# Performance work log

Measured on AMD Instinct MI355X. Metric: run time of the kernel, lower is better.

## Reference

```python
import jax, jax.numpy as jnp
import numpy as np

N, L, H, D = 8, 1024, 16, 64
HD = H * D          # hidden_size = 1024
MLP = 4 * HD        # mlp_dim = 4096
EPS = 1e-5


def _layer_norm(x, g, b):
    mu = jnp.mean(x, axis=-1, keepdims=True)
    var = jnp.var(x, axis=-1, keepdims=True)
    return (x - mu) * jax.lax.rsqrt(var + EPS) * g + b


def setup_inputs() -> dict:
    key = jax.random.key(0)
    ks = jax.random.split(key, 8)
    s_in = 1.0 / np.sqrt(HD)
    s_mlp = 1.0 / np.sqrt(MLP)
    return {
        "x": jax.random.normal(ks[0], (N, L, HD), jnp.float32),
        "ln0_g": jnp.ones((HD,), jnp.float32),
        "ln0_b": jnp.zeros((HD,), jnp.float32),
        "wq": jax.random.normal(ks[1], (HD, HD), jnp.float32) * s_in,
        "bq": jnp.zeros((HD,), jnp.float32),
        "wk": jax.random.normal(ks[2], (HD, HD), jnp.float32) * s_in,
        "bk": jnp.zeros((HD,), jnp.float32),
        "wv": jax.random.normal(ks[3], (HD, HD), jnp.float32) * s_in,
        "bv": jnp.zeros((HD,), jnp.float32),
        "wo": jax.random.normal(ks[4], (HD, HD), jnp.float32) * s_in,
        "bo": jnp.zeros((HD,), jnp.float32),
        "ln1_g": jnp.ones((HD,), jnp.float32),
        "ln1_b": jnp.zeros((HD,), jnp.float32),
        "w1": jax.random.normal(ks[5], (HD, MLP), jnp.float32) * s_in,
        "b1": jnp.zeros((MLP,), jnp.float32),
        "w2": jax.random.normal(ks[6], (MLP, HD), jnp.float32) * s_mlp,
        "b2": jnp.zeros((HD,), jnp.float32),
    }


def reference(x, ln0_g, ln0_b, wq, bq, wk, bk, wv, bv, wo, bo,
              ln1_g, ln1_b, w1, b1, w2, b2):
    n, l, hd = x.shape
    # --- pre-LN self-attention ---
    y = _layer_norm(x, ln0_g, ln0_b)
    q = (y @ wq + bq).reshape(n, l, H, D)
    k = (y @ wk + bk).reshape(n, l, H, D)
    v = (y @ wv + bv).reshape(n, l, H, D)
    qkt = jnp.einsum('nqhd,nkhd->nqkh', q, k) / jnp.sqrt(jnp.float32(D))
    attn = jax.nn.softmax(qkt, axis=2)
    y = jnp.einsum('nqkh,nkhd->nqhd', attn, v).reshape(n, l, hd)
    y = y @ wo + bo
    x = x + y  # residual (dropout_rate=0 in eval)
    # --- pre-LN MLP ---
    y = _layer_norm(x, ln1_g, ln1_b)
    y = jax.nn.gelu(y @ w1 + b1)
    y = y @ w2 + b2
    return x + y
```

## Files before the change

### kernel.cpp

```cpp
#include <hip/hip_runtime.h>
#include <math.h>

typedef __attribute__((ext_vector_type(8))) __bf16 bf16x8;
typedef __attribute__((ext_vector_type(4))) float f32x4;

#define NBATCH 8
#define SEQ    1024
#define NHEAD  16
#define DHEAD  64
#define HID    1024
#define MLPD   4096

static __device__ __forceinline__ unsigned short f2bf(float f) {
  unsigned int u = __float_as_uint(f);
  u += 0x7fffu + ((u >> 16) & 1u);
  return (unsigned short)(u >> 16);
}

static __device__ __forceinline__ void gload_lds16(const unsigned short* g,
                                                   unsigned short* l) {
  __builtin_amdgcn_global_load_lds(
      (const __attribute__((address_space(1))) unsigned int*)g,
      (__attribute__((address_space(3))) unsigned int*)l, 16, 0, 0);
}

static __device__ __forceinline__ float gelu_fast(float v) {
  const float z = 0.7978845608028654f * (v + 0.044715f * v * v * v);
  const float e = __expf(-2.0f * fabsf(z));
  float th = (1.0f - e) / (1.0f + e);
  th = copysignf(th, z);
  return 0.5f * v * (1.0f + th);
}

#define MFMA16(a, b, c) __builtin_amdgcn_mfma_f32_16x16x32_bf16(a, b, c, 0, 0, 0)

__global__ __launch_bounds__(256) void k_prep(const float* __restrict__ wq,
                                              const float* __restrict__ wk,
                                              const float* __restrict__ wv,
                                              const float* __restrict__ wo,
                                              const float* __restrict__ w1,
                                              const float* __restrict__ w2,
                                              const float* __restrict__ bq,
                                              const float* __restrict__ bk,
                                              const float* __restrict__ bv,
                                              unsigned short* __restrict__ qkvT,
                                              unsigned short* __restrict__ woT,
                                              unsigned short* __restrict__ w1T,
                                              unsigned short* __restrict__ w2T,
                                              float* __restrict__ bqkv) {
  __shared__ float t[32][33];
  const int b = blockIdx.x;
  const float* in;
  unsigned short* out;
  int R, C, ti;
  if (b < 4096) {
    const int m = b >> 10;
    ti = b & 1023; R = 1024; C = 1024;
    in  = (m == 0) ? wq : (m == 1) ? wk : (m == 2) ? wv : wo;
    out = (m == 3) ? woT : qkvT + (size_t)m * 1024 * 1024;
  } else if (b < 8192) {
    ti = b - 4096; R = 1024; C = 4096; in = w1; out = w1T;
  } else if (b < 12288) {
    ti = b - 8192; R = 4096; C = 1024; in = w2; out = w2T;
  } else {
    const int i = (b - 12288) * 256 + threadIdx.x;
    if (i < 3 * HID)
      bqkv[i] = (i < HID) ? bq[i] : (i < 2 * HID ? bk[i - HID] : bv[i - 2 * HID]);
    return;
  }
  const int tpr = C >> 5;
  const int c0 = (ti % tpr) * 32, r0 = (ti / tpr) * 32;
  const int tx = threadIdx.x & 31, ty = threadIdx.x >> 5;
#pragma unroll
  for (int j = 0; j < 4; ++j)
    t[ty + j * 8][tx] = in[(size_t)(r0 + ty + j * 8) * C + c0 + tx];
  __syncthreads();
#pragma unroll
  for (int j = 0; j < 4; ++j)
    out[(size_t)(c0 + ty + j * 8) * R + r0 + tx] = f2bf(t[tx][ty + j * 8]);
}

__global__ __launch_bounds__(256) void k_ln(const float* __restrict__ x,
                                            const float* __restrict__ gw,
                                            const float* __restrict__ bw,
                                            unsigned short* __restrict__ y) {
  __shared__ float red[2][4];
  const int row = blockIdx.x;
  const int tid = threadIdx.x;
  const float4 v = ((const float4*)(x + (size_t)row * HID))[tid];
  float sum = v.x + v.y + v.z + v.w;
  float sq  = v.x * v.x + v.y * v.y + v.z * v.z + v.w * v.w;
#pragma unroll
  for (int off = 32; off >= 1; off >>= 1) {
    sum += __shfl_xor(sum, off);
    sq  += __shfl_xor(sq, off);
  }
  if ((tid & 63) == 0) { red[0][tid >> 6] = sum; red[1][tid >> 6] = sq; }
  __syncthreads();
  sum = red[0][0] + red[0][1] + red[0][2] + red[0][3];
  sq  = red[1][0] + red[1][1] + red[1][2] + red[1][3];
  const float mu  = sum * (1.0f / HID);
  const float var = sq * (1.0f / HID) - mu * mu;
  const float rs  = rsqrtf(var + 1e-5f);
  const float4 g4 = ((const float4*)gw)[tid];
  const float4 b4 = ((const float4*)bw)[tid];
  ushort4 ov;
  ov.x = f2bf((v.x - mu) * rs * g4.x + b4.x);
  ov.y = f2bf((v.y - mu) * rs * g4.y + b4.y);
  ov.z = f2bf((v.z - mu) * rs * g4.z + b4.z);
  ov.w = f2bf((v.w - mu) * rs * g4.w + b4.w);
  ((ushort4*)(y + (size_t)row * HID))[tid] = ov;
}

template <int EPI, int BN>
__global__ __launch_bounds__(512, 2) void k_gemm(const unsigned short* __restrict__ A,
                                                 const unsigned short* __restrict__ BT,
                                                 const float* __restrict__ bias,
                                                 const float* __restrict__ res,
                                                 void* __restrict__ Cout,
                                                 int M, int N, int K) {
  constexpr int ASZ = 256 * 64;
  constexpr int BSZ = BN * 64;
  constexpr int NF  = BN / 64;
  constexpr int NCW = BN / 4;
  __shared__ unsigned short sh[2 * ASZ + 2 * BSZ];

  const int tid  = threadIdx.x;
  const int lane = tid & 63;
  const int w    = tid >> 6;
  const int wr   = w >> 2, wc = w & 3;
  const int l15  = lane & 15, g = lane >> 4;

  const int gx = gridDim.x;
  const int nwg = gx * gridDim.y;
  int lid = blockIdx.y * gx + blockIdx.x;
  lid = (lid & 7) * (nwg >> 3) + (lid >> 3);
  const int m0 = (lid / gx) * 256, n0 = (lid % gx) * BN;

  f32x4 acc[8][NF] = {};

  const int srow  = w * 8 + (lane >> 3);
  const int scolb = ((lane & 7) * 16) ^ (((lane >> 3) & 7) << 4);
  const unsigned short* pA = A  + (size_t)(m0 + srow) * K + (scolb >> 1);
  const unsigned short* pB = BT + (size_t)(n0 + srow) * K + (scolb >> 1);
  unsigned short* shB = sh + 2 * ASZ;

#define STAGE(buf_, kk)                                                     \
  do {                                                                      \
    _Pragma("unroll") for (int c = 0; c < 4; ++c)                           \
      gload_lds16(pA + (size_t)c * 64 * K + (kk),                           \
                  sh + (buf_) * ASZ + (c * 64 + w * 8) * 64);               \
    _Pragma("unroll") for (int c = 0; c < BN / 64; ++c)                     \
      gload_lds16(pB + (size_t)c * 64 * K + (kk),                           \
                  shB + (buf_) * BSZ + (c * 64 + w * 8) * 64);              \
  } while (0)

  const int fmask = (l15 & 7) << 4;
  const int bo0 = ((0 * 64) + g * 16) ^ fmask;
  const int bo1 = ((1 * 64) + g * 16) ^ fmask;
  const int aRowBase = wr * 128 + l15;
  const int bRowBase = wc * NCW + l15;

  const int NT = K >> 6;

  STAGE(0, 0);
  int buf = 0;
  for (int t = 0; t < NT; ++t) {
    const unsigned short* shAb = sh + buf * ASZ;
    const unsigned short* shBb = shB + buf * BSZ;

    asm volatile("s_waitcnt vmcnt(0)" ::: "memory");
    __builtin_amdgcn_sched_barrier(0);
    __builtin_amdgcn_s_barrier();
    if (t + 1 < NT) STAGE(buf ^ 1, (t + 1) * 64);

    bf16x8 bfr[NF][2];
#pragma unroll
    for (int n = 0; n < NF; ++n) {
      const int br = (bRowBase + n * 16) * 64;
      bfr[n][0] = *(const bf16x8*)(shBb + br + (bo0 >> 1));
      bfr[n][1] = *(const bf16x8*)(shBb + br + (bo1 >> 1));
    }
    bf16x8 afr[8][2];
#pragma unroll
    for (int m = 0; m < 8; ++m) {
      const int ar = (aRowBase + m * 16) * 64;
      afr[m][0] = *(const bf16x8*)(shAb + ar + (bo0 >> 1));
      afr[m][1] = *(const bf16x8*)(shAb + ar + (bo1 >> 1));
    }
    __builtin_amdgcn_sched_barrier(0);

#pragma unroll
    for (int p = 0; p < 4; ++p) {
#pragma unroll
      for (int n = 0; n < NF; ++n) {
        acc[2 * p][n]     = MFMA16(afr[2 * p][0],     bfr[n][0], acc[2 * p][n]);
        acc[2 * p][n]     = MFMA16(afr[2 * p][1],     bfr[n][1], acc[2 * p][n]);
        acc[2 * p + 1][n] = MFMA16(afr[2 * p + 1][0], bfr[n][0], acc[2 * p + 1][n]);
        acc[2 * p + 1][n] = MFMA16(afr[2 * p + 1][1], bfr[n][1], acc[2 * p + 1][n]);
      }
    }
    buf ^= 1;
  }
#undef STAGE

  if constexpr (EPI == 2) {
#pragma unroll
    for (int m = 0; m < 8; ++m) {
#pragma unroll
      for (int n = 0; n < NF; ++n) {
        const int col = n0 + wc * NCW + n * 16 + l15;
        const float bc = bias[col];
#pragma unroll
        for (int r = 0; r < 4; ++r) {
          const int row = m0 + wr * 128 + m * 16 + g * 4 + r;
          const size_t idx = (size_t)row * N + col;
          ((float*)Cout)[idx] = acc[m][n][r] + bc + res[idx];
        }
      }
    }
  } else {
    __builtin_amdgcn_s_barrier();
    unsigned short* ep = sh + w * (128 * NCW);
#pragma unroll
    for (int m = 0; m < 8; ++m) {
#pragma unroll
      for (int n = 0; n < NF; ++n) {
        const float bc = bias[n0 + wc * NCW + n * 16 + l15];
#pragma unroll
        for (int r = 0; r < 4; ++r) {
          float v = acc[m][n][r] + bc;
          if constexpr (EPI == 1) v = gelu_fast(v);
          ep[(m * 16 + g * 4 + r) * NCW + n * 16 + l15] = f2bf(v);
        }
      }
    }
    constexpr int CPR = NCW / 8;
#pragma unroll
    for (int j = 0; j < NCW / 4; ++j) {
      const int t = lane + j * 64;
      const int row = t / CPR, colb = (t % CPR) * 8;
      const uint4 vv = *(const uint4*)(ep + row * NCW + colb);
      unsigned short* outp = (unsigned short*)Cout +
          (size_t)(m0 + wr * 128 + row) * N + n0 + wc * NCW + colb;
      *(uint4*)outp = vv;
    }
  }
}

__global__ __launch_bounds__(256) void k_vt(const unsigned short* __restrict__ qkv,
                                            unsigned short* __restrict__ vT) {
  __shared__ unsigned short t[64][72];
  const int nh = blockIdx.y;
  const int nb = nh >> 4, h = nh & 15;
  const int l0 = blockIdx.x * 64;
  const int tx = threadIdx.x & 7;
  const int ty = threadIdx.x >> 3;
  const unsigned short* src = qkv + (size_t)(nb * SEQ + l0) * 3072 + 2048 + h * DHEAD;
#pragma unroll
  for (int j = 0; j < 2; ++j)
    *(uint4*)(&t[ty + j * 32][tx * 8]) =
        *(const uint4*)(&src[(size_t)(ty + j * 32) * 3072 + tx * 8]);
  __syncthreads();
  unsigned short* dst = vT + (size_t)nh * DHEAD * SEQ + l0;
#pragma unroll
  for (int j = 0; j < 2; ++j) {
    const int d = ty + j * 32;
    ushort4 a, b;
    a.x = t[tx * 8 + 0][d]; a.y = t[tx * 8 + 1][d];
    a.z = t[tx * 8 + 2][d]; a.w = t[tx * 8 + 3][d];
    b.x = t[tx * 8 + 4][d]; b.y = t[tx * 8 + 5][d];
    b.z = t[tx * 8 + 6][d]; b.w = t[tx * 8 + 7][d];
    *(ushort4*)(&dst[(size_t)d * SEQ + tx * 8])     = a;
    *(ushort4*)(&dst[(size_t)d * SEQ + tx * 8 + 4]) = b;
  }
}

#define SOFTMAX_GROUP(S, gq)                                                       \
  {                                                                                \
    float mx = -INFINITY;                                                          \
    _Pragma("unroll") for (int c = 0; c < 4; ++c)                                  \
      _Pragma("unroll") for (int r = 0; r < 4; ++r)                                \
        mx = fmaxf(mx, S[c][r]);                                                   \
    mx = fmaxf(mx, __shfl_xor(mx, 16));                                            \
    mx = fmaxf(mx, __shfl_xor(mx, 32));                                            \
    const float mnew = fmaxf(m_run[gq], mx);                                       \
    const float sc = __expf(0.125f * (m_run[gq] - mnew));                          \
    m_run[gq] = mnew;                                                              \
    float ts = 0.0f;                                                               \
    _Pragma("unroll") for (int c = 0; c < 4; ++c) {                                \
      const float p0 = __expf(0.125f * (S[c][0] - mnew));                          \
      const float p1 = __expf(0.125f * (S[c][1] - mnew));                          \
      const float p2 = __expf(0.125f * (S[c][2] - mnew));                          \
      const float p3 = __expf(0.125f * (S[c][3] - mnew));                          \
      ts += (p0 + p1) + (p2 + p3);                                                 \
      const unsigned int lo = (unsigned int)f2bf(p0) | ((unsigned int)f2bf(p1) << 16); \
      const unsigned int hi = (unsigned int)f2bf(p2) | ((unsigned int)f2bf(p3) << 16); \
      *(uint2*)(&P_lds[w][((gq) * 16 + l15) * 72 + c * 16 + g * 4]) = make_uint2(lo, hi); \
    }                                                                              \
    ts += __shfl_xor(ts, 16);                                                      \
    ts += __shfl_xor(ts, 32);                                                      \
    s_run[gq] = s_run[gq] * sc + ts;                                               \
    const float scr0 = __shfl(sc, g * 4 + 0), scr1 = __shfl(sc, g * 4 + 1);        \
    const float scr2 = __shfl(sc, g * 4 + 2), scr3 = __shfl(sc, g * 4 + 3);        \
    _Pragma("unroll") for (int dt = 0; dt < 4; ++dt) {                             \
      o[gq][dt][0] *= scr0; o[gq][dt][1] *= scr1;                                  \
      o[gq][dt][2] *= scr2; o[gq][dt][3] *= scr3;                                  \
    }                                                                              \
  }

__global__ __launch_bounds__(256, 4) void k_attn(const unsigned short* __restrict__ qkv,
                                                 const unsigned short* __restrict__ vT,
                                                 unsigned short* __restrict__ outp) {
  __shared__ unsigned short Ks[64 * 64];
  __shared__ unsigned short Vs[64 * 64];
  __shared__ unsigned short P_lds[4][32 * 72];
  const int tid  = threadIdx.x;
  const int lane = tid & 63;
  const int w    = tid >> 6;
  const int l15  = lane & 15, g = lane >> 4;
  const int nh = blockIdx.y;
  const int nb = nh >> 4, h = nh & 15;
  const int q0 = blockIdx.x * 128 + w * 32;
  const size_t RS = 3 * HID;

  const unsigned short* Qp = qkv + (size_t)(nb * SEQ + q0) * RS + h * DHEAD;
  const unsigned short* Kg = qkv + (size_t)(nb * SEQ) * RS + HID + h * DHEAD;
  const unsigned short* Vg = vT + (size_t)nh * DHEAD * SEQ;

  const int L0 = tid * 32, L1 = L0 + 16;
  const int kr0 = L0 >> 7, kc0 = (L0 & 127) ^ ((kr0 & 7) << 4);
  const int kr1 = L1 >> 7, kc1 = (L1 & 127) ^ ((kr1 & 7) << 4);

  bf16x8 aq[2][2];
#pragma unroll
  for (int gq = 0; gq < 2; ++gq)
#pragma unroll
    for (int t = 0; t < 2; ++t)
      aq[gq][t] = *(const bf16x8*)(&Qp[(size_t)(gq * 16 + l15) * RS + t * 32 + g * 8]);

  f32x4 o[2][4] = {};
  float m_run[2] = {-INFINITY, -INFINITY};
  float s_run[2] = {0.0f, 0.0f};

  uint4 rk0, rk1, rv0, rv1;
  rk0 = *(const uint4*)(Kg + (size_t)kr0 * RS + (kc0 >> 1));
  rk1 = *(const uint4*)(Kg + (size_t)kr1 * RS + (kc1 >> 1));
  rv0 = *(const uint4*)(Vg + (size_t)kr0 * SEQ + (kc0 >> 1));
  rv1 = *(const uint4*)(Vg + (size_t)kr1 * SEQ + (kc1 >> 1));
  *(uint4*)(&Ks[tid * 16])     = rk0;
  *(uint4*)(&Ks[tid * 16 + 8]) = rk1;
  *(uint4*)(&Vs[tid * 16])     = rv0;
  *(uint4*)(&Vs[tid * 16 + 8]) = rv1;
  __syncthreads();

  const int sw = (l15 & 7) << 4;

  for (int t16 = 0; t16 < 16; ++t16) {
    if (t16 < 15) {
      const int kb = (t16 + 1) * 64;
      rk0 = *(const uint4*)(Kg + (size_t)(kb + kr0) * RS + (kc0 >> 1));
      rk1 = *(const uint4*)(Kg + (size_t)(kb + kr1) * RS + (kc1 >> 1));
      rv0 = *(const uint4*)(Vg + (size_t)kr0 * SEQ + kb + (kc0 >> 1));
      rv1 = *(const uint4*)(Vg + (size_t)kr1 * SEQ + kb + (kc1 >> 1));
    }

    f32x4 S0[4], S1[4];
#pragma unroll
    for (int c = 0; c < 4; ++c) {
      const int krow = c * 16 + l15;
      const bf16x8 k0 = *(const bf16x8*)(&Ks[krow * 64 + ((( 0 + g * 16) ^ sw) >> 1)]);
      const bf16x8 k1 = *(const bf16x8*)(&Ks[krow * 64 + (((64 + g * 16) ^ sw) >> 1)]);
      f32x4 a = {};
      a = MFMA16(k0, aq[0][0], a);
      a = MFMA16(k1, aq[0][1], a);
      S0[c] = a;
      f32x4 b = {};
      b = MFMA16(k0, aq[1][0], b);
      b = MFMA16(k1, aq[1][1], b);
      S1[c] = b;
    }

    SOFTMAX_GROUP(S0, 0)
    SOFTMAX_GROUP(S1, 1)

    bf16x8 pa[2][2];
#pragma unroll
    for (int gq = 0; gq < 2; ++gq)
#pragma unroll
      for (int th = 0; th < 2; ++th)
        pa[gq][th] = *(const bf16x8*)(&P_lds[w][(gq * 16 + l15) * 72 + th * 32 + g * 8]);
#pragma unroll
    for (int dt = 0; dt < 4; ++dt) {
      const int vrow = dt * 16 + l15;
      const bf16x8 v0 = *(const bf16x8*)(&Vs[vrow * 64 + ((( 0 + g * 16) ^ sw) >> 1)]);
      const bf16x8 v1 = *(const bf16x8*)(&Vs[vrow * 64 + (((64 + g * 16) ^ sw) >> 1)]);
      o[0][dt] = MFMA16(pa[0][0], v0, o[0][dt]);
      o[0][dt] = MFMA16(pa[0][1], v1, o[0][dt]);
      o[1][dt] = MFMA16(pa[1][0], v0, o[1][dt]);
      o[1][dt] = MFMA16(pa[1][1], v1, o[1][dt]);
    }
    __syncthreads();
    if (t16 < 15) {
      *(uint4*)(&Ks[tid * 16])     = rk0;
      *(uint4*)(&Ks[tid * 16 + 8]) = rk1;
      *(uint4*)(&Vs[tid * 16])     = rv0;
      *(uint4*)(&Vs[tid * 16 + 8]) = rv1;
      __syncthreads();
    }
  }

#pragma unroll
  for (int gq = 0; gq < 2; ++gq) {
    float sr[4];
#pragma unroll
    for (int r = 0; r < 4; ++r) sr[r] = 1.0f / __shfl(s_run[gq], g * 4 + r);
#pragma unroll
    for (int dt = 0; dt < 4; ++dt)
#pragma unroll
      for (int r = 0; r < 4; ++r)
        outp[(size_t)(nb * SEQ + q0 + gq * 16 + g * 4 + r) * HID + h * DHEAD + dt * 16 + l15] =
            f2bf(o[gq][dt][r] * sr[r]);
  }
}

extern "C" void kernel_launch(void* const* d_in, const int* in_sizes, int n_in,
                              void* d_out, int out_size, void* d_ws, size_t ws_size,
                              hipStream_t stream) {
  const float* x    = (const float*)d_in[0];
  const float* ln0g = (const float*)d_in[1];
  const float* ln0b = (const float*)d_in[2];
  const float* wq   = (const float*)d_in[3];
  const float* bq   = (const float*)d_in[4];
  const float* wk   = (const float*)d_in[5];
  const float* bk   = (const float*)d_in[6];
  const float* wv   = (const float*)d_in[7];
  const float* bv   = (const float*)d_in[8];
  const float* wo   = (const float*)d_in[9];
  const float* bo   = (const float*)d_in[10];
  const float* ln1g = (const float*)d_in[11];
  const float* ln1b = (const float*)d_in[12];
  const float* w1   = (const float*)d_in[13];
  const float* b1   = (const float*)d_in[14];
  const float* w2   = (const float*)d_in[15];
  const float* b2   = (const float*)d_in[16];
  float* out = (float*)d_out;

  char* ws = (char*)d_ws;
  unsigned short* qkvT = (unsigned short*)(ws + 0);
  unsigned short* woT  = (unsigned short*)(ws + 6291456);
  unsigned short* w1T  = (unsigned short*)(ws + 8388608);
  unsigned short* w2T  = (unsigned short*)(ws + 16777216);
  float*          bqkv = (float*)(ws + 25165824);
  unsigned short* ybuf = (unsigned short*)(ws + 25178112);
  unsigned short* qkv  = (unsigned short*)(ws + 41955328);
  unsigned short* att  = (unsigned short*)(ws + 92286976);
  unsigned short* hbuf = qkv;
  unsigned short* vT   = ybuf;

  const int M = NBATCH * SEQ;

  k_prep<<<dim3(12300), 256, 0, stream>>>(wq, wk, wv, wo, w1, w2, bq, bk, bv,
                                          qkvT, woT, w1T, w2T, bqkv);

  k_ln<<<dim3(M), 256, 0, stream>>>(x, ln0g, ln0b, ybuf);
  k_gemm<0, 256><<<dim3(12, 32), 512, 0, stream>>>(ybuf, qkvT, bqkv, nullptr, (void*)qkv, M, 3 * HID, HID);
  k_vt<<<dim3(16, 128), 256, 0, stream>>>(qkv, vT);
  k_attn<<<dim3(8, 128), 256, 0, stream>>>(qkv, vT, att);
  k_gemm<2, 128><<<dim3(8, 32), 512, 0, stream>>>(att, woT, bo, x, (void*)out, M, HID, HID);
  k_ln<<<dim3(M), 256, 0, stream>>>(out, ln1g, ln1b, ybuf);
  k_gemm<1, 256><<<dim3(16, 32), 512, 0, stream>>>(ybuf, w1T, b1, nullptr, (void*)hbuf, M, MLPD, HID);
  k_gemm<2, 128><<<dim3(8, 32), 512, 0, stream>>>(hbuf, w2T, b2, out, (void*)out, M, HID, MLPD);
}
```

Baseline: 363.6 us.

## Shrink GEMM tiles to 256x128 with K-step 32 for higher occupancy

The GEMM kernel now uses a fixed 256x128 output tile and a K-step of 32 instead of 64, which cuts shared memory per block and raises the launch-bounds occupancy target from 2 to 4 blocks. The swizzled LDS staging, fragment loads and epilogue staging are rewritten to match, with the epilogue split into two 64-row halves. The QKV and MLP-up grids double in the N direction. The aim is more resident workgroups to hide latency, at the cost of less data reuse per tile and twice as many barrier/load iterations along K.

```diff
diff --git a/kernel.cpp b/kernel.cpp
--- a/kernel.cpp
+++ b/kernel.cpp
@@ -112,17 +112,18 @@
   ((ushort4*)(y + (size_t)row * HID))[tid] = ov;
 }
 
-template <int EPI, int BN>
-__global__ __launch_bounds__(512, 2) void k_gemm(const unsigned short* __restrict__ A,
+template <int EPI>
+__global__ __launch_bounds__(512, 4) void k_gemm(const unsigned short* __restrict__ A,
                                                  const unsigned short* __restrict__ BT,
                                                  const float* __restrict__ bias,
                                                  const float* __restrict__ res,
                                                  void* __restrict__ Cout,
                                                  int M, int N, int K) {
-  constexpr int ASZ = 256 * 64;
-  constexpr int BSZ = BN * 64;
-  constexpr int NF  = BN / 64;
-  constexpr int NCW = BN / 4;
+  constexpr int BN  = 128;
+  constexpr int ASZ = 256 * 32;
+  constexpr int BSZ = BN * 32;
+  constexpr int NF  = 2;
+  constexpr int NCW = 32;
   __shared__ unsigned short sh[2 * ASZ + 2 * BSZ];
 
   const int tid  = threadIdx.x;
@@ -139,29 +140,24 @@
 
   f32x4 acc[8][NF] = {};
 
-  const int srow  = w * 8 + (lane >> 3);
-  const int scolb = ((lane & 7) * 16) ^ (((lane >> 3) & 7) << 4);
-  const unsigned short* pA = A  + (size_t)(m0 + srow) * K + (scolb >> 1);
-  const unsigned short* pB = BT + (size_t)(n0 + srow) * K + (scolb >> 1);
+  const int srow4 = lane >> 2;
+  const int schk  = (lane & 3) ^ ((lane >> 3) & 3);
+  const unsigned short* pA = A  + (size_t)(m0 + w * 32 + srow4) * K + schk * 8;
+  const unsigned short* pB = BT + (size_t)(n0 + w * 16 + srow4) * K + schk * 8;
   unsigned short* shB = sh + 2 * ASZ;
 
-#define STAGE(buf_, kk)                                                     \
-  do {                                                                      \
-    _Pragma("unroll") for (int c = 0; c < 4; ++c)                           \
-      gload_lds16(pA + (size_t)c * 64 * K + (kk),                           \
-                  sh + (buf_) * ASZ + (c * 64 + w * 8) * 64);               \
-    _Pragma("unroll") for (int c = 0; c < BN / 64; ++c)                     \
-      gload_lds16(pB + (size_t)c * 64 * K + (kk),                           \
-                  shB + (buf_) * BSZ + (c * 64 + w * 8) * 64);              \
+#define STAGE(buf_, kk)                                                      \
+  do {                                                                       \
+    gload_lds16(pA + (kk),                  sh  + (buf_) * ASZ + (w * 32) * 32);      \
+    gload_lds16(pA + (size_t)16 * K + (kk), sh  + (buf_) * ASZ + (w * 32 + 16) * 32); \
+    gload_lds16(pB + (kk),                  shB + (buf_) * BSZ + (w * 16) * 32);      \
   } while (0)
 
-  const int fmask = (l15 & 7) << 4;
-  const int bo0 = ((0 * 64) + g * 16) ^ fmask;
-  const int bo1 = ((1 * 64) + g * 16) ^ fmask;
+  const int fko = (g ^ ((l15 >> 1) & 3)) * 8;
   const int aRowBase = wr * 128 + l15;
   const int bRowBase = wc * NCW + l15;
 
-  const int NT = K >> 6;
+  const int NT = K >> 5;
 
   STAGE(0, 0);
   int buf = 0;
@@ -172,32 +168,24 @@
     asm volatile("s_waitcnt vmcnt(0)" ::: "memory");
     __builtin_amdgcn_sched_barrier(0);
     __builtin_amdgcn_s_barrier();
-    if (t + 1 < NT) STAGE(buf ^ 1, (t + 1) * 64);
-
-    bf16x8 bfr[NF][2];
-#pragma unroll
-    for (int n = 0; n < NF; ++n) {
-      const int br = (bRowBase + n * 16) * 64;
-      bfr[n][0] = *(const bf16x8*)(shBb + br + (bo0 >> 1));
-      bfr[n][1] = *(const bf16x8*)(shBb + br + (bo1 >> 1));
-    }
-    bf16x8 afr[8][2];
-#pragma unroll
-    for (int m = 0; m < 8; ++m) {
-      const int ar = (aRowBase + m * 16) * 64;
-      afr[m][0] = *(const bf16x8*)(shAb + ar + (bo0 >> 1));
-      afr[m][1] = *(const bf16x8*)(shAb + ar + (bo1 >> 1));
-    }
+    if (t + 1 < NT) STAGE(buf ^ 1, (t + 1) * 32);
+
+    bf16x8 bfr[NF];
+#pragma unroll
+    for (int n = 0; n < NF; ++n)
+      bfr[n] = *(const bf16x8*)(shBb + (bRowBase + n * 16) * 32 + fko);
+    bf16x8 afr[8];
+#pragma unroll
+    for (int m = 0; m < 8; ++m)
+      afr[m] = *(const bf16x8*)(shAb + (aRowBase + m * 16) * 32 + fko);
     __builtin_amdgcn_sched_barrier(0);
 
 #pragma unroll
     for (int p = 0; p < 4; ++p) {
 #pragma unroll
       for (int n = 0; n < NF; ++n) {
-        acc[2 * p][n]     = MFMA16(afr[2 * p][0],     bfr[n][0], acc[2 * p][n]);
-        acc[2 * p][n]     = MFMA16(afr[2 * p][1],     bfr[n][1], acc[2 * p][n]);
-        acc[2 * p + 1][n] = MFMA16(afr[2 * p + 1][0], bfr[n][0], acc[2 * p + 1][n]);
-        acc[2 * p + 1][n] = MFMA16(afr[2 * p + 1][1], bfr[n][1], acc[2 * p + 1][n]);
+        acc[2 * p][n]     = MFMA16(afr[2 * p],     bfr[n], acc[2 * p][n]);
+        acc[2 * p + 1][n] = MFMA16(afr[2 * p + 1], bfr[n], acc[2 * p + 1][n]);
       }
     }
     buf ^= 1;
@@ -221,29 +209,32 @@
     }
   } else {
     __builtin_amdgcn_s_barrier();
-    unsigned short* ep = sh + w * (128 * NCW);
-#pragma unroll
-    for (int m = 0; m < 8; ++m) {
-#pragma unroll
-      for (int n = 0; n < NF; ++n) {
-        const float bc = bias[n0 + wc * NCW + n * 16 + l15];
-#pragma unroll
-        for (int r = 0; r < 4; ++r) {
-          float v = acc[m][n][r] + bc;
-          if constexpr (EPI == 1) v = gelu_fast(v);
-          ep[(m * 16 + g * 4 + r) * NCW + n * 16 + l15] = f2bf(v);
+    unsigned short* ep = sh + w * (64 * NCW);
+#pragma unroll
+    for (int hm = 0; hm < 2; ++hm) {
+#pragma unroll
+      for (int m = 0; m < 4; ++m) {
+        const int mm = hm * 4 + m;
+#pragma unroll
+        for (int n = 0; n < NF; ++n) {
+          const float bc = bias[n0 + wc * NCW + n * 16 + l15];
+#pragma unroll
+          for (int r = 0; r < 4; ++r) {
+            float v = acc[mm][n][r] + bc;
+            if constexpr (EPI == 1) v = gelu_fast(v);
+            ep[(m * 16 + g * 4 + r) * NCW + n * 16 + l15] = f2bf(v);
+          }
         }
       }
-    }
-    constexpr int CPR = NCW / 8;
-#pragma unroll
-    for (int j = 0; j < NCW / 4; ++j) {
-      const int t = lane + j * 64;
-      const int row = t / CPR, colb = (t % CPR) * 8;
-      const uint4 vv = *(const uint4*)(ep + row * NCW + colb);
-      unsigned short* outp = (unsigned short*)Cout +
-          (size_t)(m0 + wr * 128 + row) * N + n0 + wc * NCW + colb;
-      *(uint4*)outp = vv;
+#pragma unroll
+      for (int j = 0; j < 4; ++j) {
+        const int t = lane + j * 64;
+        const int row = t >> 2, colb = (t & 3) * 8;
+        const uint4 vv = *(const uint4*)(ep + row * NCW + colb);
+        unsigned short* outp = (unsigned short*)Cout +
+            (size_t)(m0 + wr * 128 + hm * 64 + row) * N + n0 + wc * NCW + colb;
+        *(uint4*)outp = vv;
+      }
     }
   }
 }
@@ -464,11 +455,11 @@
                                           qkvT, woT, w1T, w2T, bqkv);
 
   k_ln<<<dim3(M), 256, 0, stream>>>(x, ln0g, ln0b, ybuf);
-  k_gemm<0, 256><<<dim3(12, 32), 512, 0, stream>>>(ybuf, qkvT, bqkv, nullptr, (void*)qkv, M, 3 * HID, HID);
+  k_gemm<0><<<dim3(24, 32), 512, 0, stream>>>(ybuf, qkvT, bqkv, nullptr, (void*)qkv, M, 3 * HID, HID);
   k_vt<<<dim3(16, 128), 256, 0, stream>>>(qkv, vT);
   k_attn<<<dim3(8, 128), 256, 0, stream>>>(qkv, vT, att);
-  k_gemm<2, 128><<<dim3(8, 32), 512, 0, stream>>>(att, woT, bo, x, (void*)out, M, HID, HID);
+  k_gemm<2><<<dim3(8, 32), 512, 0, stream>>>(att, woT, bo, x, (void*)out, M, HID, HID);
   k_ln<<<dim3(M), 256, 0, stream>>>(out, ln1g, ln1b, ybuf);
-  k_gemm<1, 256><<<dim3(16, 32), 512, 0, stream>>>(ybuf, w1T, b1, nullptr, (void*)hbuf, M, MLPD, HID);
-  k_gemm<2, 128><<<dim3(8, 32), 512, 0, stream>>>(hbuf, w2T, b2, out, (void*)out, M, HID, MLPD);
-}
+  k_gemm<1><<<dim3(32, 32), 512, 0, stream>>>(ybuf, w1T, b1, nullptr, (void*)hbuf, M, MLPD, HID);
+  k_gemm<2><<<dim3(8, 32), 512, 0, stream>>>(hbuf, w2T, b2, out, (void*)out, M, HID, MLPD);
+}
```

Result: slower. 384.2 us (+5.7%).

## Add K=32 GEMM kernel with higher occupancy for QKV, out-proj, MLP1

Applied to the files above, without the earlier changes.

Adds a new GEMM variant with a 256x128 tile and a K-step of 32. Its smaller LDS footprint and new swizzle allow four workgroups per CU. The QKV and MLP-up GEMMs switch from BN=256 to BN=128 tiles, doubling their grid size, and the out-projection also uses the new kernel. The MLP-down GEMM keeps the K=64 variant. The cost is more barriers per unit of K and lower data reuse per tile, in exchange for more waves to hide latency.

```diff
diff --git a/kernel.cpp b/kernel.cpp
--- a/kernel.cpp
+++ b/kernel.cpp
@@ -112,17 +112,18 @@
   ((ushort4*)(y + (size_t)row * HID))[tid] = ov;
 }
 
-template <int EPI, int BN>
-__global__ __launch_bounds__(512, 2) void k_gemm(const unsigned short* __restrict__ A,
-                                                 const unsigned short* __restrict__ BT,
-                                                 const float* __restrict__ bias,
-                                                 const float* __restrict__ res,
-                                                 void* __restrict__ Cout,
-                                                 int M, int N, int K) {
-  constexpr int ASZ = 256 * 64;
-  constexpr int BSZ = BN * 64;
-  constexpr int NF  = BN / 64;
-  constexpr int NCW = BN / 4;
+template <int EPI>
+__global__ __launch_bounds__(512, 4) void k_g32(const unsigned short* __restrict__ A,
+                                                const unsigned short* __restrict__ BT,
+                                                const float* __restrict__ bias,
+                                                const float* __restrict__ res,
+                                                void* __restrict__ Cout,
+                                                int M, int N, int K) {
+  constexpr int BN  = 128;
+  constexpr int ASZ = 256 * 32;
+  constexpr int BSZ = BN * 32;
+  constexpr int NF  = 2;
+  constexpr int NCW = 32;
   __shared__ unsigned short sh[2 * ASZ + 2 * BSZ];
 
   const int tid  = threadIdx.x;
@@ -139,13 +140,140 @@
 
   f32x4 acc[8][NF] = {};
 
+  const int srow4 = lane >> 2;
+  const int schk  = (lane & 3) ^ ((lane >> 3) & 3);
+  const unsigned short* pA = A  + (size_t)(m0 + w * 32 + srow4) * K + schk * 8;
+  const unsigned short* pB = BT + (size_t)(n0 + w * 16 + srow4) * K + schk * 8;
+  unsigned short* shB = sh + 2 * ASZ;
+
+#define STAGE32(buf_, kk)                                                     \
+  do {                                                                        \
+    gload_lds16(pA + (kk),                  sh  + (buf_) * ASZ + (w * 32) * 32);      \
+    gload_lds16(pA + (size_t)16 * K + (kk), sh  + (buf_) * ASZ + (w * 32 + 16) * 32); \
+    gload_lds16(pB + (kk),                  shB + (buf_) * BSZ + (w * 16) * 32);      \
+  } while (0)
+
+  const int fko = (g ^ ((l15 >> 1) & 3)) * 8;
+  const int aRowBase = wr * 128 + l15;
+  const int bRowBase = wc * NCW + l15;
+
+  const int NT = K >> 5;
+
+  STAGE32(0, 0);
+  int buf = 0;
+  for (int t = 0; t < NT; ++t) {
+    const unsigned short* shAb = sh + buf * ASZ;
+    const unsigned short* shBb = shB + buf * BSZ;
+
+    asm volatile("s_waitcnt vmcnt(0)" ::: "memory");
+    __builtin_amdgcn_sched_barrier(0);
+    __builtin_amdgcn_s_barrier();
+    if (t + 1 < NT) STAGE32(buf ^ 1, (t + 1) * 32);
+
+    bf16x8 bfr[NF];
+#pragma unroll
+    for (int n = 0; n < NF; ++n)
+      bfr[n] = *(const bf16x8*)(shBb + (bRowBase + n * 16) * 32 + fko);
+    bf16x8 afr[8];
+#pragma unroll
+    for (int m = 0; m < 8; ++m)
+      afr[m] = *(const bf16x8*)(shAb + (aRowBase + m * 16) * 32 + fko);
+    __builtin_amdgcn_sched_barrier(0);
+
+#pragma unroll
+    for (int p = 0; p < 4; ++p) {
+#pragma unroll
+      for (int n = 0; n < NF; ++n) {
+        acc[2 * p][n]     = MFMA16(afr[2 * p],     bfr[n], acc[2 * p][n]);
+        acc[2 * p + 1][n] = MFMA16(afr[2 * p + 1], bfr[n], acc[2 * p + 1][n]);
+      }
+    }
+    buf ^= 1;
+  }
+#undef STAGE32
+
+  if constexpr (EPI == 2) {
+#pragma unroll
+    for (int m = 0; m < 8; ++m) {
+#pragma unroll
+      for (int n = 0; n < NF; ++n) {
+        const int col = n0 + wc * NCW + n * 16 + l15;
+        const float bc = bias[col];
+#pragma unroll
+        for (int r = 0; r < 4; ++r) {
+          const int row = m0 + wr * 128 + m * 16 + g * 4 + r;
+          const size_t idx = (size_t)row * N + col;
+          ((float*)Cout)[idx] = acc[m][n][r] + bc + res[idx];
+        }
+      }
+    }
+  } else {
+    __builtin_amdgcn_s_barrier();
+    unsigned short* ep = sh + w * (64 * NCW);
+#pragma unroll
+    for (int hm = 0; hm < 2; ++hm) {
+#pragma unroll
+      for (int m = 0; m < 4; ++m) {
+        const int mm = hm * 4 + m;
+#pragma unroll
+        for (int n = 0; n < NF; ++n) {
+          const float bc = bias[n0 + wc * NCW + n * 16 + l15];
+#pragma unroll
+          for (int r = 0; r < 4; ++r) {
+            float v = acc[mm][n][r] + bc;
+            if constexpr (EPI == 1) v = gelu_fast(v);
+            ep[(m * 16 + g * 4 + r) * NCW + n * 16 + l15] = f2bf(v);
+          }
+        }
+      }
+#pragma unroll
+      for (int j = 0; j < 4; ++j) {
+        const int t = lane + j * 64;
+        const int row = t >> 2, colb = (t & 3) * 8;
+        const uint4 vv = *(const uint4*)(ep + row * NCW + colb);
+        unsigned short* outp = (unsigned short*)Cout +
+            (size_t)(m0 + wr * 128 + hm * 64 + row) * N + n0 + wc * NCW + colb;
+        *(uint4*)outp = vv;
+      }
+    }
+  }
+}
+
+template <int EPI>
+__global__ __launch_bounds__(512, 2) void k_g64(const unsigned short* __restrict__ A,
+                                                const unsigned short* __restrict__ BT,
+                                                const float* __restrict__ bias,
+                                                const float* __restrict__ res,
+                                                void* __restrict__ Cout,
+                                                int M, int N, int K) {
+  constexpr int BN  = 128;
+  constexpr int ASZ = 256 * 64;
+  constexpr int BSZ = BN * 64;
+  constexpr int NF  = 2;
+  constexpr int NCW = 32;
+  __shared__ unsigned short sh[2 * ASZ + 2 * BSZ];
+
+  const int tid  = threadIdx.x;
+  const int lane = tid & 63;
+  const int w    = tid >> 6;
+  const int wr   = w >> 2, wc = w & 3;
+  const int l15  = lane & 15, g = lane >> 4;
+
+  const int gx = gridDim.x;
+  const int nwg = gx * gridDim.y;
+  int lid = blockIdx.y * gx + blockIdx.x;
+  lid = (lid & 7) * (nwg >> 3) + (lid >> 3);
+  const int m0 = (lid / gx) * 256, n0 = (lid % gx) * BN;
+
+  f32x4 acc[8][NF] = {};
+
   const int srow  = w * 8 + (lane >> 3);
   const int scolb = ((lane & 7) * 16) ^ (((lane >> 3) & 7) << 4);
   const unsigned short* pA = A  + (size_t)(m0 + srow) * K + (scolb >> 1);
   const unsigned short* pB = BT + (size_t)(n0 + srow) * K + (scolb >> 1);
   unsigned short* shB = sh + 2 * ASZ;
 
-#define STAGE(buf_, kk)                                                     \
+#define STAGE64(buf_, kk)                                                   \
   do {                                                                      \
     _Pragma("unroll") for (int c = 0; c < 4; ++c)                           \
       gload_lds16(pA + (size_t)c * 64 * K + (kk),                           \
@@ -163,7 +291,7 @@
 
   const int NT = K >> 6;
 
-  STAGE(0, 0);
+  STAGE64(0, 0);
   int buf = 0;
   for (int t = 0; t < NT; ++t) {
     const unsigned short* shAb = sh + buf * ASZ;
@@ -172,7 +300,7 @@
     asm volatile("s_waitcnt vmcnt(0)" ::: "memory");
     __builtin_amdgcn_sched_barrier(0);
     __builtin_amdgcn_s_barrier();
-    if (t + 1 < NT) STAGE(buf ^ 1, (t + 1) * 64);
+    if (t + 1 < NT) STAGE64(buf ^ 1, (t + 1) * 64);
 
     bf16x8 bfr[NF][2];
 #pragma unroll
@@ -202,7 +330,7 @@
     }
     buf ^= 1;
   }
-#undef STAGE
+#undef STAGE64
 
   if constexpr (EPI == 2) {
 #pragma unroll
@@ -464,11 +592,11 @@
                                           qkvT, woT, w1T, w2T, bqkv);
 
   k_ln<<<dim3(M), 256, 0, stream>>>(x, ln0g, ln0b, ybuf);
-  k_gemm<0, 256><<<dim3(12, 32), 512, 0, stream>>>(ybuf, qkvT, bqkv, nullptr, (void*)qkv, M, 3 * HID, HID);
+  k_g32<0><<<dim3(24, 32), 512, 0, stream>>>(ybuf, qkvT, bqkv, nullptr, (void*)qkv, M, 3 * HID, HID);
   k_vt<<<dim3(16, 128), 256, 0, stream>>>(qkv, vT);
   k_attn<<<dim3(8, 128), 256, 0, stream>>>(qkv, vT, att);
-  k_gemm<2, 128><<<dim3(8, 32), 512, 0, stream>>>(att, woT, bo, x, (void*)out, M, HID, HID);
+  k_g32<2><<<dim3(8, 32), 512, 0, stream>>>(att, woT, bo, x, (void*)out, M, HID, HID);
   k_ln<<<dim3(M), 256, 0, stream>>>(out, ln1g, ln1b, ybuf);
-  k_gemm<1, 256><<<dim3(16, 32), 512, 0, stream>>>(ybuf, w1T, b1, nullptr, (void*)hbuf, M, MLPD, HID);
-  k_gemm<2, 128><<<dim3(8, 32), 512, 0, stream>>>(hbuf, w2T, b2, out, (void*)out, M, HID, MLPD);
-}
+  k_g32<1><<<dim3(32, 32), 512, 0, stream>>>(ybuf, w1T, b1, nullptr, (void*)hbuf, M, MLPD, HID);
+  k_g64<2><<<dim3(8, 32), 512, 0, stream>>>(hbuf, w2T, b2, out, (void*)out, M, HID, MLPD);
+}
```

Measured after the change: 364.4 us. About the same (+0.2%).
